# Kernel optimization log

Measured on AMD Instinct MI355X. Metric: run time of the kernel, lower is better.

The kernel has to match this reference:

```python
import jax, jax.numpy as jnp
import numpy as np

B, T, D_MEM, D_Q, D_ATT, C_LOC, K = 64, 2000, 512, 1024, 128, 32, 31


def setup_inputs() -> dict:
    key = jax.random.key(0)
    ks = jax.random.split(key, 9)
    return {
        "attention_hidden_state": jax.random.normal(ks[0], (B, 1, D_Q), jnp.float32),
        "memory": jax.random.normal(ks[1], (B, T, D_MEM), jnp.float32),
        "processed_memory": jax.random.normal(ks[2], (B, T, D_ATT), jnp.float32),
        "attention_weights": jax.random.uniform(ks[3], (B, 2, T), jnp.float32),
        "Wq": jax.random.normal(ks[4], (D_Q, D_ATT), jnp.float32) * 0.02,
        "Wconv": jax.random.normal(ks[5], (C_LOC, 2, K), jnp.float32) * 0.1,
        "bconv": jax.random.normal(ks[6], (C_LOC,), jnp.float32) * 0.01,
        "Wloc": jax.random.normal(ks[7], (C_LOC, D_ATT), jnp.float32) * 0.1,
        "v": jax.random.normal(ks[8], (D_ATT,), jnp.float32) * 0.1,
    }


def reference(attention_hidden_state, memory, processed_memory, attention_weights,
              Wq, Wconv, bconv, Wloc, v):
    # query projection: [B,1,1024] @ [1024,128] -> [B,1,128]
    processed_query = jnp.einsum("bqi,io->bqo", attention_hidden_state, Wq)
    # location conv: [B,2,T] -> [B,32,T], 'same' padding (k=31, pad=15)
    loc = jax.lax.conv_general_dilated(
        attention_weights, Wconv, window_strides=(1,), padding=[(15, 15)],
        dimension_numbers=("NCH", "OIH", "NCH"))
    loc = loc + bconv[None, :, None]
    # transpose to [B,T,32] then project to [B,T,128]
    processed_loc = jnp.einsum("bct,co->bto", loc, Wloc)
    # energies: v . tanh(q + loc + mem) -> [B,T]
    energies = jnp.einsum("btd,d->bt", jnp.tanh(processed_query + processed_loc + processed_memory), v)
    new_weights = jax.nn.softmax(energies, axis=1)
    # context: [B,T] x [B,T,D] -> [B,D]
    attention_context = jnp.einsum("bt,btd->bd", new_weights, memory)
    return attention_context, new_weights
```

## Files before the change

### kernel.cpp

```cpp
#include <hip/hip_runtime.h>
#include <hip/hip_bf16.h>

#define B 64
#define T 2000
#define D_MEM 512
#define D_Q 1024
#define D_ATT 128
#define C_LOC 32
#define K 31

#define WS_PQ       0
#define WS_ENERGY   (WS_PQ + B*D_ATT)
#define NCHUNK      10
#define TCHUNK      (T / NCHUNK)
#define WS_PARTIAL  (WS_ENERGY + B*T)

__device__ __forceinline__ float tanh_fast(float x) {
    float e = __expf(2.f * x);
    return 1.f - 2.f / (e + 1.f);
}

__global__ void pq_kernel(const float* __restrict__ h, const float* __restrict__ Wq,
                          float* __restrict__ pq) {
    int b = blockIdx.x;
    int d = threadIdx.x;
    __shared__ float sh[D_Q];
    const float* hb = h + (size_t)b * D_Q;
    for (int i = threadIdx.x; i < D_Q / 4; i += 128)
        ((float4*)sh)[i] = ((const float4*)hb)[i];
    __syncthreads();
    float acc = 0.f;
#pragma unroll 8
    for (int i = 0; i < D_Q; ++i)
        acc = fmaf(sh[i], Wq[(size_t)i * D_ATT + d], acc);
    pq[b * D_ATT + d] = acc;
}

#define CH 16
__global__ void energy_kernel(const float* __restrict__ aw,
                              const float* __restrict__ pmem,
                              const float* __restrict__ pq,
                              const float* __restrict__ Wconv,
                              const float* __restrict__ bconv,
                              const float* __restrict__ Wloc,
                              const float* __restrict__ v,
                              float* __restrict__ energies) {
    const int b  = blockIdx.y;
    const int t0 = blockIdx.x * CH;
    const int tid = threadIdx.x;

    __shared__ float s_aw[2][CH + K - 1];
    __shared__ float s_wc[2 * K * C_LOC];
    __shared__ float s_loc[CH][C_LOC];
    __shared__ float s_pq[D_ATT];

    for (int j = tid; j < 2 * (CH + K - 1); j += 256) {
        int i = j / (CH + K - 1), o = j % (CH + K - 1);
        int t = t0 - (K / 2) + o;
        s_aw[i][o] = (t >= 0 && t < T) ? aw[((size_t)b * 2 + i) * T + t] : 0.f;
    }
    for (int j = tid; j < C_LOC * 2 * K; j += 256) {
        int c = j / (2 * K), r = j % (2 * K);
        int i = r / K, k = r % K;
        s_wc[(i * K + k) * C_LOC + c] = Wconv[j];
    }
    if (tid < D_ATT) s_pq[tid] = pq[b * D_ATT + tid];
    __syncthreads();

    {
        int tt = tid >> 5, c = tid & 31;
        float bc = bconv[c];
        float acc0 = bc, acc1 = bc;
#pragma unroll
        for (int i = 0; i < 2; ++i) {
#pragma unroll
            for (int k = 0; k < K; ++k) {
                float wv = s_wc[(i * K + k) * C_LOC + c];
                acc0 = fmaf(s_aw[i][tt + k],     wv, acc0);
                acc1 = fmaf(s_aw[i][tt + 8 + k], wv, acc1);
            }
        }
        s_loc[tt][c] = acc0;
        s_loc[tt + 8][c] = acc1;
    }
    __syncthreads();

    int tt = tid >> 5, dd = tid & 31;
    float4 pqv = ((const float4*)s_pq)[dd];
    float4 vv  = ((const float4*)v)[dd];
#pragma unroll
    for (int iter = 0; iter < 2; ++iter) {
        int ts = iter * 8 + tt;
        int t = t0 + ts;
        float4 pm = ((const float4*)(pmem + ((size_t)b * T + t) * D_ATT))[dd];
        float4 pl = {0.f, 0.f, 0.f, 0.f};
#pragma unroll
        for (int c = 0; c < C_LOC; ++c) {
            float l = s_loc[ts][c];
            float4 w = ((const float4*)(Wloc + c * D_ATT))[dd];
            pl.x = fmaf(l, w.x, pl.x);
            pl.y = fmaf(l, w.y, pl.y);
            pl.z = fmaf(l, w.z, pl.z);
            pl.w = fmaf(l, w.w, pl.w);
        }
        float e = vv.x * tanh_fast(pqv.x + pl.x + pm.x)
                + vv.y * tanh_fast(pqv.y + pl.y + pm.y)
                + vv.z * tanh_fast(pqv.z + pl.z + pm.z)
                + vv.w * tanh_fast(pqv.w + pl.w + pm.w);
#pragma unroll
        for (int off = 16; off >= 1; off >>= 1)
            e += __shfl_xor(e, off);
        if (dd == 0) energies[(size_t)b * T + t] = e;
    }
}

__global__ void softmax_kernel(const float* __restrict__ energies,
                               float* __restrict__ weights) {
    int b = blockIdx.x, tid = threadIdx.x;
    const float* e = energies + (size_t)b * T;
    float vals[8];
    float m = -1e30f;
#pragma unroll
    for (int j = 0; j < 8; ++j) {
        int t = j * 256 + tid;
        vals[j] = (t < T) ? e[t] : -1e30f;
        m = fmaxf(m, vals[j]);
    }
    __shared__ float smax[4], ssum[4];
    int wid = tid >> 6, lane = tid & 63;
#pragma unroll
    for (int off = 32; off >= 1; off >>= 1) m = fmaxf(m, __shfl_xor(m, off));
    if (lane == 0) smax[wid] = m;
    __syncthreads();
    m = fmaxf(fmaxf(smax[0], smax[1]), fmaxf(smax[2], smax[3]));

    float s = 0.f;
#pragma unroll
    for (int j = 0; j < 8; ++j) {
        int t = j * 256 + tid;
        vals[j] = (t < T) ? __expf(vals[j] - m) : 0.f;
        s += vals[j];
    }
#pragma unroll
    for (int off = 32; off >= 1; off >>= 1) s += __shfl_xor(s, off);
    if (lane == 0) ssum[wid] = s;
    __syncthreads();
    s = ssum[0] + ssum[1] + ssum[2] + ssum[3];
    float inv = 1.f / s;
#pragma unroll
    for (int j = 0; j < 8; ++j) {
        int t = j * 256 + tid;
        if (t < T) weights[(size_t)b * T + t] = vals[j] * inv;
    }
}

__global__ void ctx_partial_kernel(const float* __restrict__ memory,
                                   const float* __restrict__ weights,
                                   float* __restrict__ partial) {
    int b = blockIdx.y, s = blockIdx.x;
    int dq = threadIdx.x;
    int tbeg = s * TCHUNK;
    __shared__ float sw[TCHUNK];
    const float* w = weights + (size_t)b * T;
    for (int j = threadIdx.x; j < TCHUNK; j += 128) sw[j] = w[tbeg + j];
    __syncthreads();
    const float4* mem4 = (const float4*)(memory + (size_t)b * T * D_MEM);
    float4 acc = {0.f, 0.f, 0.f, 0.f};
#pragma unroll 8
    for (int j = 0; j < TCHUNK; ++j) {
        float wt = sw[j];
        float4 mv = mem4[(size_t)(tbeg + j) * (D_MEM / 4) + dq];
        acc.x = fmaf(wt, mv.x, acc.x);
        acc.y = fmaf(wt, mv.y, acc.y);
        acc.z = fmaf(wt, mv.z, acc.z);
        acc.w = fmaf(wt, mv.w, acc.w);
    }
    ((float4*)(partial + ((size_t)s * B + b) * D_MEM))[dq] = acc;
}

__global__ void ctx_reduce_kernel(const float* __restrict__ partial,
                                  float* __restrict__ ctx) {
    int idx = blockIdx.x * 256 + threadIdx.x;
    float acc = 0.f;
#pragma unroll
    for (int s = 0; s < NCHUNK; ++s)
        acc += partial[(size_t)s * B * D_MEM + idx];
    ctx[idx] = acc;
}

extern "C" void kernel_launch(void* const* d_in, const int* in_sizes, int n_in,
                              void* d_out, int out_size, void* d_ws, size_t ws_size,
                              hipStream_t stream) {
    const float* hidden = (const float*)d_in[0];
    const float* memory = (const float*)d_in[1];
    const float* pmem   = (const float*)d_in[2];
    const float* aw     = (const float*)d_in[3];
    const float* Wq     = (const float*)d_in[4];
    const float* Wconv  = (const float*)d_in[5];
    const float* bconv  = (const float*)d_in[6];
    const float* Wloc   = (const float*)d_in[7];
    const float* v      = (const float*)d_in[8];

    float* out_ctx = (float*)d_out;
    float* out_w   = (float*)d_out + B * D_MEM;

    float* ws       = (float*)d_ws;
    float* pq       = ws + WS_PQ;
    float* energies = ws + WS_ENERGY;
    float* partial  = ws + WS_PARTIAL;

    pq_kernel<<<B, 128, 0, stream>>>(hidden, Wq, pq);
    energy_kernel<<<dim3(T / CH, B), 256, 0, stream>>>(aw, pmem, pq, Wconv, bconv,
                                                       Wloc, v, energies);
    softmax_kernel<<<B, 256, 0, stream>>>(energies, out_w);
    ctx_partial_kernel<<<dim3(NCHUNK, B), 128, 0, stream>>>(memory, out_w, partial);
    ctx_reduce_kernel<<<(B * D_MEM) / 256, 256, 0, stream>>>(partial, out_ctx);
}
```

Measured before the change: 544.7 us.

## Split pq reduction across warps, widen energy tiles, double ctx chunks

The query projection now splits its 1024-long dot product across four 128-thread groups and sums the partials in shared memory, giving each block more parallelism. The energy kernel processes 40 timesteps per block with 5 per thread, so each Wloc load is reused across several timesteps and the conv window halo is amortised. The context pass uses 20 chunks instead of 10 to launch more blocks, and launch bounds are added everywhere. In exchange the energy kernel holds more registers, has fewer blocks, and the context reduce reads twice as many partials.

```diff
diff --git a/kernel.cpp b/kernel.cpp
--- a/kernel.cpp
+++ b/kernel.cpp
@@ -11,7 +11,7 @@
 
 #define WS_PQ       0
 #define WS_ENERGY   (WS_PQ + B*D_ATT)
-#define NCHUNK      10
+#define NCHUNK      20
 #define TCHUNK      (T / NCHUNK)
 #define WS_PARTIAL  (WS_ENERGY + B*T)
 
@@ -20,24 +20,34 @@
     return 1.f - 2.f / (e + 1.f);
 }
 
-__global__ void pq_kernel(const float* __restrict__ h, const float* __restrict__ Wq,
-                          float* __restrict__ pq) {
+__global__ __launch_bounds__(512) void pq_kernel(const float* __restrict__ h,
+                                                 const float* __restrict__ Wq,
+                                                 float* __restrict__ pq) {
     int b = blockIdx.x;
-    int d = threadIdx.x;
+    int tid = threadIdx.x;
+    int ty = tid >> 7;
+    int d  = tid & 127;
     __shared__ float sh[D_Q];
+    __shared__ float red[4][D_ATT];
     const float* hb = h + (size_t)b * D_Q;
-    for (int i = threadIdx.x; i < D_Q / 4; i += 128)
-        ((float4*)sh)[i] = ((const float4*)hb)[i];
+    if (tid < D_Q / 4) ((float4*)sh)[tid] = ((const float4*)hb)[tid];
     __syncthreads();
     float acc = 0.f;
+    int ibeg = ty * 256;
 #pragma unroll 8
-    for (int i = 0; i < D_Q; ++i)
+    for (int i2 = 0; i2 < 256; ++i2) {
+        int i = ibeg + i2;
         acc = fmaf(sh[i], Wq[(size_t)i * D_ATT + d], acc);
-    pq[b * D_ATT + d] = acc;
-}
-
-#define CH 16
-__global__ void energy_kernel(const float* __restrict__ aw,
+    }
+    red[ty][d] = acc;
+    __syncthreads();
+    if (ty == 0)
+        pq[b * D_ATT + d] = red[0][d] + red[1][d] + red[2][d] + red[3][d];
+}
+
+#define CH 40
+#define TPT 5
+__global__ __launch_bounds__(256) void energy_kernel(const float* __restrict__ aw,
                               const float* __restrict__ pmem,
                               const float* __restrict__ pq,
                               const float* __restrict__ Wconv,
@@ -68,45 +78,52 @@
     __syncthreads();
 
     {
-        int tt = tid >> 5, c = tid & 31;
+        int g = tid >> 5, c = tid & 31;
         float bc = bconv[c];
-        float acc0 = bc, acc1 = bc;
+        float acc[TPT];
+#pragma unroll
+        for (int j = 0; j < TPT; ++j) acc[j] = bc;
 #pragma unroll
         for (int i = 0; i < 2; ++i) {
 #pragma unroll
             for (int k = 0; k < K; ++k) {
                 float wv = s_wc[(i * K + k) * C_LOC + c];
-                acc0 = fmaf(s_aw[i][tt + k],     wv, acc0);
-                acc1 = fmaf(s_aw[i][tt + 8 + k], wv, acc1);
+#pragma unroll
+                for (int j = 0; j < TPT; ++j)
+                    acc[j] = fmaf(s_aw[i][g + 8 * j + k], wv, acc[j]);
             }
         }
-        s_loc[tt][c] = acc0;
-        s_loc[tt + 8][c] = acc1;
-    }
-    __syncthreads();
-
-    int tt = tid >> 5, dd = tid & 31;
+#pragma unroll
+        for (int j = 0; j < TPT; ++j) s_loc[g + 8 * j][c] = acc[j];
+    }
+    __syncthreads();
+
+    int g = tid >> 5, dd = tid & 31;
     float4 pqv = ((const float4*)s_pq)[dd];
     float4 vv  = ((const float4*)v)[dd];
-#pragma unroll
-    for (int iter = 0; iter < 2; ++iter) {
-        int ts = iter * 8 + tt;
-        int t = t0 + ts;
+    float4 pl[TPT];
+#pragma unroll
+    for (int j = 0; j < TPT; ++j) pl[j] = make_float4(0.f, 0.f, 0.f, 0.f);
+#pragma unroll
+    for (int c = 0; c < C_LOC; ++c) {
+        float4 w = ((const float4*)(Wloc + c * D_ATT))[dd];
+#pragma unroll
+        for (int j = 0; j < TPT; ++j) {
+            float l = s_loc[g + 8 * j][c];
+            pl[j].x = fmaf(l, w.x, pl[j].x);
+            pl[j].y = fmaf(l, w.y, pl[j].y);
+            pl[j].z = fmaf(l, w.z, pl[j].z);
+            pl[j].w = fmaf(l, w.w, pl[j].w);
+        }
+    }
+#pragma unroll
+    for (int j = 0; j < TPT; ++j) {
+        int t = t0 + g + 8 * j;
         float4 pm = ((const float4*)(pmem + ((size_t)b * T + t) * D_ATT))[dd];
-        float4 pl = {0.f, 0.f, 0.f, 0.f};
-#pragma unroll
-        for (int c = 0; c < C_LOC; ++c) {
-            float l = s_loc[ts][c];
-            float4 w = ((const float4*)(Wloc + c * D_ATT))[dd];
-            pl.x = fmaf(l, w.x, pl.x);
-            pl.y = fmaf(l, w.y, pl.y);
-            pl.z = fmaf(l, w.z, pl.z);
-            pl.w = fmaf(l, w.w, pl.w);
-        }
-        float e = vv.x * tanh_fast(pqv.x + pl.x + pm.x)
-                + vv.y * tanh_fast(pqv.y + pl.y + pm.y)
-                + vv.z * tanh_fast(pqv.z + pl.z + pm.z)
-                + vv.w * tanh_fast(pqv.w + pl.w + pm.w);
+        float e = vv.x * tanh_fast(pqv.x + pl[j].x + pm.x)
+                + vv.y * tanh_fast(pqv.y + pl[j].y + pm.y)
+                + vv.z * tanh_fast(pqv.z + pl[j].z + pm.z)
+                + vv.w * tanh_fast(pqv.w + pl[j].w + pm.w);
 #pragma unroll
         for (int off = 16; off >= 1; off >>= 1)
             e += __shfl_xor(e, off);
@@ -114,7 +131,7 @@
     }
 }
 
-__global__ void softmax_kernel(const float* __restrict__ energies,
+__global__ __launch_bounds__(256) void softmax_kernel(const float* __restrict__ energies,
                                float* __restrict__ weights) {
     int b = blockIdx.x, tid = threadIdx.x;
     const float* e = energies + (size_t)b * T;
@@ -154,7 +171,7 @@
     }
 }
 
-__global__ void ctx_partial_kernel(const float* __restrict__ memory,
+__global__ __launch_bounds__(128) void ctx_partial_kernel(const float* __restrict__ memory,
                                    const float* __restrict__ weights,
                                    float* __restrict__ partial) {
     int b = blockIdx.y, s = blockIdx.x;
@@ -166,7 +183,7 @@
     __syncthreads();
     const float4* mem4 = (const float4*)(memory + (size_t)b * T * D_MEM);
     float4 acc = {0.f, 0.f, 0.f, 0.f};
-#pragma unroll 8
+#pragma unroll 10
     for (int j = 0; j < TCHUNK; ++j) {
         float wt = sw[j];
         float4 mv = mem4[(size_t)(tbeg + j) * (D_MEM / 4) + dq];
@@ -178,7 +195,7 @@
     ((float4*)(partial + ((size_t)s * B + b) * D_MEM))[dq] = acc;
 }
 
-__global__ void ctx_reduce_kernel(const float* __restrict__ partial,
+__global__ __launch_bounds__(256) void ctx_reduce_kernel(const float* __restrict__ partial,
                                   float* __restrict__ ctx) {
     int idx = blockIdx.x * 256 + threadIdx.x;
     float acc = 0.f;
@@ -209,7 +226,7 @@
     float* energies = ws + WS_ENERGY;
     float* partial  = ws + WS_PARTIAL;
 
-    pq_kernel<<<B, 128, 0, stream>>>(hidden, Wq, pq);
+    pq_kernel<<<B, 512, 0, stream>>>(hidden, Wq, pq);
     energy_kernel<<<dim3(T / CH, B), 256, 0, stream>>>(aw, pmem, pq, Wconv, bconv,
                                                        Wloc, v, energies);
     softmax_kernel<<<B, 256, 0, stream>>>(energies, out_w);
```

After: 523.0 us. -4.0%, faster.
